# Kernel tuning notes

Hardware: AMD Instinct MI355X
Metric: run time of the kernel (lower is better)

Reference implementation:

```python
import jax, jax.numpy as jnp
import numpy as np
from jax import lax

B, T, E, K = 64, 512, 2048, 32


def setup_inputs() -> dict:
    key = jax.random.key(0)
    ks = jax.random.split(key, 8)
    X = jax.random.normal(ks[0], (B, T, E), dtype=jnp.float32)
    y = jax.random.randint(ks[1], (B, T), 0, K, dtype=jnp.int32)
    # variable-length mask: lengths in [T//2, T], position 0 always valid
    lengths = jax.random.randint(ks[2], (B,), T // 2, T + 1)
    mask = (jnp.arange(T)[None, :] < lengths[:, None])
    W = jax.random.normal(ks[3], (E, K), dtype=jnp.float32) * 0.02
    b = jnp.zeros((K,), dtype=jnp.float32)
    transitions = jax.random.normal(ks[4], (K, K), dtype=jnp.float32) * 0.1
    start_transitions = jax.random.normal(ks[5], (K,), dtype=jnp.float32) * 0.1
    end_transitions = jax.random.normal(ks[6], (K,), dtype=jnp.float32) * 0.1
    return {"X": X, "y": y, "mask": mask, "W": W, "b": b,
            "transitions": transitions,
            "start_transitions": start_transitions,
            "end_transitions": end_transitions}


def _input_likelihood(logits, mask, trans, start, end):
    # forward algorithm (log partition), AllenNLP semantics
    lt = jnp.transpose(logits, (1, 0, 2))  # [T,B,K]
    mt = mask.T                            # [T,B]
    alpha0 = start[None, :] + lt[0]        # [B,K]

    def step(alpha, xm):
        x, m = xm  # x:[B,K], m:[B]
        inner = alpha[:, :, None] + trans[None, :, :] + x[:, None, :]  # [B,K,K]
        new = jax.nn.logsumexp(inner, axis=1)
        return jnp.where(m[:, None], new, alpha), None

    alpha, _ = lax.scan(step, alpha0, (lt[1:], mt[1:]))
    return jax.nn.logsumexp(alpha + end[None, :], axis=1)  # [B]


def _joint_likelihood(logits, tags, mask, trans, start, end):
    maskf = mask.astype(logits.dtype)
    emit = jnp.take_along_axis(logits, tags[:, :, None], axis=2)[:, :, 0]  # [B,T]
    emit_score = jnp.sum(emit * maskf, axis=1)
    trans_sc = trans[tags[:, :-1], tags[:, 1:]]  # [B,T-1]
    trans_score = jnp.sum(trans_sc * maskf[:, 1:], axis=1)
    lengths = jnp.sum(mask.astype(jnp.int32), axis=1)
    last_tags = jnp.take_along_axis(tags, (lengths - 1)[:, None], axis=1)[:, 0]
    return start[tags[:, 0]] + emit_score + trans_score + end[last_tags]


def reference(X, y, mask, W, b, transitions, start_transitions, end_transitions):
    logits = jnp.einsum('bte,ek->btk', X, W) + b  # projection
    log_num = _joint_likelihood(logits, y, mask, transitions,
                                start_transitions, end_transitions)
    log_den = _input_likelihood(logits, mask, transitions,
                                start_transitions, end_transitions)
    # CRF.forward training path: loss = -crf(inputs, tags, mask)
    return -jnp.sum(log_num - log_den)
```

## Files before the change

kernel.cpp:

```cpp
#include <hip/hip_runtime.h>

#define Bn 64
#define Tn 512
#define En 2048
#define Kn 32
#define Mn (Bn*Tn)
#define LOG2E 1.4426950408889634f
#define LN2   0.6931471805599453f

typedef __attribute__((ext_vector_type(8))) short short8;
typedef __attribute__((ext_vector_type(4))) float floatx4;

__device__ inline unsigned int pack_bf16(float a, float b) {
    unsigned int ua = __float_as_uint(a), ub = __float_as_uint(b);
    return ((ua + 0x8000u) >> 16) | (((ub + 0x8000u) & 0xFFFF0000u));
}

__device__ inline float rdlane(float v, int l) {
    return __uint_as_float(__builtin_amdgcn_readlane(__float_as_uint(v), l));
}

__global__ __launch_bounds__(256) void prep_kernel(const float* __restrict__ W,
                                                   unsigned short* __restrict__ Wt,
                                                   float* __restrict__ out) {
    int idx = blockIdx.x * 256 + threadIdx.x;
    int k = idx >> 11, e = idx & 2047;
    float w = W[e * Kn + k];
    Wt[idx] = (unsigned short)((__float_as_uint(w) + 0x8000u) >> 16);
    if (idx == 0) out[0] = 0.f;
}

__global__ __launch_bounds__(256) void gemm_kernel(const float* __restrict__ X,
                                                   const float* __restrict__ bias,
                                                   const unsigned short* __restrict__ Wt,
                                                   float* __restrict__ logits2) {
    const int tid  = threadIdx.x;
    const int wave = tid >> 6;
    const int lane = tid & 63;
    const int ml   = lane & 15;
    const int quad = lane >> 4;
    const int row0 = blockIdx.x * 64;

    const float*          xp  = X  + (size_t)(row0 + wave * 16 + ml) * En + quad * 8;
    const unsigned short* b0p = Wt + ml * En        + quad * 8;
    const unsigned short* b1p = Wt + (16 + ml) * En + quad * 8;

    floatx4 acc0 = {0.f,0.f,0.f,0.f};
    floatx4 acc1 = {0.f,0.f,0.f,0.f};

    #pragma unroll 4
    for (int e0 = 0; e0 < En; e0 += 32) {
        float4 xa = *(const float4*)(xp + e0);
        float4 xb = *(const float4*)(xp + e0 + 4);
        short8 b0 = *(const short8*)(b0p + e0);
        short8 b1 = *(const short8*)(b1p + e0);
        union { unsigned int u[4]; short8 s; } av;
        av.u[0] = pack_bf16(xa.x, xa.y);
        av.u[1] = pack_bf16(xa.z, xa.w);
        av.u[2] = pack_bf16(xb.x, xb.y);
        av.u[3] = pack_bf16(xb.z, xb.w);
        acc0 = __builtin_amdgcn_mfma_f32_16x16x32_bf16(av.s, b0, acc0, 0, 0, 0);
        acc1 = __builtin_amdgcn_mfma_f32_16x16x32_bf16(av.s, b1, acc1, 0, 0, 0);
    }

    const float bc0 = bias[ml], bc1 = bias[16 + ml];
    const int gr = row0 + wave * 16 + quad * 4;
    #pragma unroll
    for (int r = 0; r < 4; ++r) {
        logits2[(size_t)(gr + r) * Kn + ml]      = (acc0[r] + bc0) * LOG2E;
        logits2[(size_t)(gr + r) * Kn + 16 + ml] = (acc1[r] + bc1) * LOG2E;
    }
}

__global__ __launch_bounds__(64) void crf_kernel(const float* __restrict__ logits2,
                                                 const int* __restrict__ y,
                                                 const void* __restrict__ maskp,
                                                 const float* __restrict__ trans,
                                                 const float* __restrict__ start,
                                                 const float* __restrict__ endt,
                                                 float* __restrict__ out) {
    const int b    = blockIdx.x;
    const int lane = threadIdx.x;
    const int j    = lane & 31;

    unsigned int first = *(const unsigned int*)maskp;
    int mode;
    if (first <= 1u) mode = 0;
    else if (first == 0x3F800000u) mode = 2;
    else mode = 1;

    int len = 0;
    if (mode == 0) {
        const int* mb = (const int*)maskp + b * Tn;
        for (int t = lane; t < Tn; t += 64) len += (mb[t] != 0);
    } else if (mode == 1) {
        const unsigned char* mb = (const unsigned char*)maskp + b * Tn;
        for (int t = lane; t < Tn; t += 64) len += (mb[t] != 0);
    } else {
        const float* mb = (const float*)maskp + b * Tn;
        for (int t = lane; t < Tn; t += 64) len += (mb[t] != 0.f);
    }
    #pragma unroll
    for (int o = 32; o; o >>= 1) len += __shfl_xor(len, o, 64);

    const int* yb = y + b * Tn;
    float num2 = 0.f;
    for (int t = lane; t < Tn; t += 64) {
        if (t < len) {
            int yt = yb[t];
            num2 += logits2[((size_t)b * Tn + t) * Kn + yt];
            if (t >= 1) num2 += trans[yb[t - 1] * Kn + yt] * LOG2E;
        }
    }
    if (lane == 0) num2 += (start[yb[0]] + endt[yb[len - 1]]) * LOG2E;
    #pragma unroll
    for (int o = 32; o; o >>= 1) num2 += __shfl_xor(num2, o, 64);

    float P[32];
    #pragma unroll
    for (int i = 0; i < 32; ++i)
        P[i] = __builtin_exp2f(trans[i * Kn + j] * LOG2E);

    const float* xrow = logits2 + (size_t)b * Tn * Kn;
    float a = start[j] * LOG2E + xrow[j];
    float S = 0.f;

    float cur[4], nxt[4];
    #pragma unroll
    for (int q = 0; q < 4; ++q) {
        int tq = 1 + q; if (tq > Tn - 1) tq = Tn - 1;
        cur[q] = xrow[tq * Kn + j];
    }

    for (int g = 1; g < len; g += 4) {
        #pragma unroll
        for (int q = 0; q < 4; ++q) {
            int tq = g + 4 + q; if (tq > Tn - 1) tq = Tn - 1;
            nxt[q] = xrow[tq * Kn + j];
        }
        #pragma unroll
        for (int q = 0; q < 4; ++q) {
            if (g + q < len) {
                float u = __builtin_exp2f(a);
                float w0 = 0.f, w1 = 0.f, w2 = 0.f, w3 = 0.f;
                #pragma unroll
                for (int i = 0; i < 32; i += 4) {
                    float s0 = rdlane(u, i);
                    float s1 = rdlane(u, i + 1);
                    float s2 = rdlane(u, i + 2);
                    float s3 = rdlane(u, i + 3);
                    w0 = fmaf(s0, P[i],     w0);
                    w1 = fmaf(s1, P[i + 1], w1);
                    w2 = fmaf(s2, P[i + 2], w2);
                    w3 = fmaf(s3, P[i + 3], w3);
                }
                float w = (w0 + w1) + (w2 + w3);
                float n = cur[q] + __builtin_log2f(w);
                if (q == 3) {
                    float sg = rdlane(n, 0);
                    a = n - sg;
                    S += sg;
                } else {
                    a = n;
                }
            }
        }
        #pragma unroll
        for (int q = 0; q < 4; ++q) cur[q] = nxt[q];
    }

    float v = (lane < 32) ? __builtin_exp2f(a + endt[j] * LOG2E) : 0.f;
    #pragma unroll
    for (int o = 32; o; o >>= 1) v += __shfl_xor(v, o, 64);
    float den2 = S + __builtin_log2f(v);

    if (lane == 0) atomicAdd(out, (den2 - num2) * LN2);
}

extern "C" void kernel_launch(void* const* d_in, const int* in_sizes, int n_in,
                              void* d_out, int out_size, void* d_ws, size_t ws_size,
                              hipStream_t stream) {
    const float* X     = (const float*)d_in[0];
    const int*   y     = (const int*)  d_in[1];
    const void*  mask  =               d_in[2];
    const float* W     = (const float*)d_in[3];
    const float* bias  = (const float*)d_in[4];
    const float* trans = (const float*)d_in[5];
    const float* start = (const float*)d_in[6];
    const float* endt  = (const float*)d_in[7];
    float* out = (float*)d_out;

    float* logits2 = (float*)d_ws;
    unsigned short* Wt = (unsigned short*)((char*)d_ws + (size_t)Mn * Kn * 4);

    prep_kernel<<<256, 256, 0, stream>>>(W, Wt, out);
    gemm_kernel<<<Mn / 64, 256, 0, stream>>>(X, bias, Wt, logits2);
    crf_kernel<<<Bn, 64, 0, stream>>>(logits2, y, mask, trans, start, endt, out);
}
```

Measured before the change: 466.7 us.

## Parallelize CRF forward recursion over time segments via MFMA transfer-matrix products

Splits each sequence's forward recursion into 8 segments of 64 steps. Each segment computes the product of its per-step 32x32 transfer matrices with bf16 MFMA, applying periodic exponent rescaling, and a combine kernel chains the segment matrices into the alpha vector. This turns a serial 512-step chain over 64 blocks into 512 blocks each running a shorter chain, exposing more parallelism. The cost is extra matrix-product work and bf16 truncation of intermediate products, which may affect accuracy. The GEMM unroll is also raised from 4 to 8.

```diff
diff --git a/kernel.cpp b/kernel.cpp
--- a/kernel.cpp
+++ b/kernel.cpp
@@ -7,15 +7,20 @@
 #define Mn (Bn*Tn)
 #define LOG2E 1.4426950408889634f
 #define LN2   0.6931471805599453f
-
-typedef __attribute__((ext_vector_type(8))) short short8;
-typedef __attribute__((ext_vector_type(4))) float floatx4;
+#define NSEG 8
+#define SEGLEN 64
+
+typedef __attribute__((ext_vector_type(8)))  short short8;
+typedef __attribute__((ext_vector_type(4)))  float floatx4;
+typedef __attribute__((ext_vector_type(16))) float floatx16;
 
 __device__ inline unsigned int pack_bf16(float a, float b) {
     unsigned int ua = __float_as_uint(a), ub = __float_as_uint(b);
     return ((ua + 0x8000u) >> 16) | (((ub + 0x8000u) & 0xFFFF0000u));
 }
-
+__device__ inline unsigned int pack_trunc(float lo, float hi) {
+    return (__float_as_uint(lo) >> 16) | (__float_as_uint(hi) & 0xFFFF0000u);
+}
 __device__ inline float rdlane(float v, int l) {
     return __uint_as_float(__builtin_amdgcn_readlane(__float_as_uint(v), l));
 }
@@ -48,7 +53,7 @@
     floatx4 acc0 = {0.f,0.f,0.f,0.f};
     floatx4 acc1 = {0.f,0.f,0.f,0.f};
 
-    #pragma unroll 4
+    #pragma unroll 8
     for (int e0 = 0; e0 < En; e0 += 32) {
         float4 xa = *(const float4*)(xp + e0);
         float4 xb = *(const float4*)(xp + e0 + 4);
@@ -72,23 +77,9 @@
     }
 }
 
-__global__ __launch_bounds__(64) void crf_kernel(const float* __restrict__ logits2,
-                                                 const int* __restrict__ y,
-                                                 const void* __restrict__ maskp,
-                                                 const float* __restrict__ trans,
-                                                 const float* __restrict__ start,
-                                                 const float* __restrict__ endt,
-                                                 float* __restrict__ out) {
-    const int b    = blockIdx.x;
-    const int lane = threadIdx.x;
-    const int j    = lane & 31;
-
+__device__ inline int seq_len(const void* maskp, int b, int lane) {
     unsigned int first = *(const unsigned int*)maskp;
-    int mode;
-    if (first <= 1u) mode = 0;
-    else if (first == 0x3F800000u) mode = 2;
-    else mode = 1;
-
+    int mode = (first <= 1u) ? 0 : (first == 0x3F800000u ? 2 : 1);
     int len = 0;
     if (mode == 0) {
         const int* mb = (const int*)maskp + b * Tn;
@@ -102,6 +93,124 @@
     }
     #pragma unroll
     for (int o = 32; o; o >>= 1) len += __shfl_xor(len, o, 64);
+    return len;
+}
+
+__global__ __launch_bounds__(64) void crf_seg_kernel(const float* __restrict__ logits2,
+                                                     const void* __restrict__ maskp,
+                                                     const float* __restrict__ trans,
+                                                     float* __restrict__ Hs,
+                                                     float* __restrict__ Ss) {
+    const int bx = blockIdx.x;
+    const int b = bx >> 3, s = bx & 7;
+    const int lane = threadIdx.x;
+    const int j = lane & 31;
+    const int h = lane >> 5;
+
+    const int len = seq_len(maskp, b, lane);
+    if (s * SEGLEN >= len) return;
+    const int tstart = (s == 0) ? 1 : s * SEGLEN;
+    const int tend   = min(s * SEGLEN + SEGLEN - 1, len - 1);
+
+    float PT1[8], PT2[8];
+    #pragma unroll
+    for (int i = 0; i < 8; ++i) {
+        PT1[i] = __builtin_exp2f(trans[(8 * h + i) * Kn + j] * LOG2E);
+        PT2[i] = __builtin_exp2f(trans[(16 + 8 * h + i) * Kn + j] * LOG2E);
+    }
+
+    union U4 { unsigned int u[4]; short8 v; };
+    U4 fb1, fb2;
+    #pragma unroll
+    for (int p = 0; p < 4; ++p) { fb1.u[p] = 0u; fb2.u[p] = 0u; }
+    int i1 = j - 8 * h;
+    if (i1 >= 0 && i1 < 8) fb1.u[i1 >> 1] |= 0x3F80u << (16 * (i1 & 1));
+    int i2 = j - 16 - 8 * h;
+    if (i2 >= 0 && i2 < 8) fb2.u[i2 >> 1] |= 0x3F80u << (16 * (i2 & 1));
+
+    const float* xrow = logits2 + (size_t)b * Tn * Kn + j;
+    floatx16 Hc;
+    float S = 0.f;
+    int stepc = 0;
+
+    float cur[4], nxt[4];
+    #pragma unroll
+    for (int q = 0; q < 4; ++q) cur[q] = xrow[min(tstart + q, tend) * Kn];
+
+    for (int g = tstart; g <= tend; g += 4) {
+        #pragma unroll
+        for (int q = 0; q < 4; ++q) nxt[q] = xrow[min(g + 4 + q, tend) * Kn];
+        #pragma unroll
+        for (int q = 0; q < 4; ++q) {
+            if (g + q <= tend) {
+                float e = __builtin_exp2f(cur[q]);
+                U4 fa1, fa2;
+                #pragma unroll
+                for (int p = 0; p < 4; ++p) {
+                    fa1.u[p] = pack_trunc(e * PT1[2 * p], e * PT1[2 * p + 1]);
+                    fa2.u[p] = pack_trunc(e * PT2[2 * p], e * PT2[2 * p + 1]);
+                }
+                floatx16 acc = {0.f,0.f,0.f,0.f,0.f,0.f,0.f,0.f,
+                                0.f,0.f,0.f,0.f,0.f,0.f,0.f,0.f};
+                acc = __builtin_amdgcn_mfma_f32_32x32x16_bf16(fa1.v, fb1.v, acc, 0, 0, 0);
+                acc = __builtin_amdgcn_mfma_f32_32x32x16_bf16(fa2.v, fb2.v, acc, 0, 0, 0);
+
+                if ((stepc & 7) == 7) {
+                    float m = acc[0];
+                    #pragma unroll
+                    for (int r = 1; r < 16; ++r) m = fmaxf(m, acc[r]);
+                    #pragma unroll
+                    for (int o = 1; o < 64; o <<= 1) m = fmaxf(m, __shfl_xor(m, o, 64));
+                    int eb = (int)((__float_as_uint(m) >> 23) & 0xFF);
+                    float scale = __uint_as_float((unsigned int)(254 - eb) << 23);
+                    #pragma unroll
+                    for (int r = 0; r < 16; ++r) acc[r] *= scale;
+                    S += (float)(eb - 127);
+                }
+                ++stepc;
+                Hc = acc;
+
+                unsigned int w[8], pw[8];
+                #pragma unroll
+                for (int p = 0; p < 8; ++p) w[p] = pack_trunc(acc[2 * p], acc[2 * p + 1]);
+                #pragma unroll
+                for (int p = 0; p < 8; ++p) pw[p] = __shfl_xor(w[p], 32, 64);
+                if (h == 0) {
+                    fb1.u[0] = w[0];  fb1.u[1] = w[1];  fb1.u[2] = pw[0]; fb1.u[3] = pw[1];
+                    fb2.u[0] = w[4];  fb2.u[1] = w[5];  fb2.u[2] = pw[4]; fb2.u[3] = pw[5];
+                } else {
+                    fb1.u[0] = pw[2]; fb1.u[1] = pw[3]; fb1.u[2] = w[2];  fb1.u[3] = w[3];
+                    fb2.u[0] = pw[6]; fb2.u[1] = pw[7]; fb2.u[2] = w[6];  fb2.u[3] = w[7];
+                }
+            }
+        }
+        #pragma unroll
+        for (int q = 0; q < 4; ++q) cur[q] = nxt[q];
+    }
+
+    float* hp = Hs + (size_t)(b * 8 + s) * 1024;
+    #pragma unroll
+    for (int r = 0; r < 16; ++r) {
+        int row = (r & 3) + 8 * (r >> 2) + 4 * h;
+        hp[row * 32 + j] = Hc[r];
+    }
+    if (lane == 0) Ss[b * 8 + s] = S;
+}
+
+__global__ __launch_bounds__(64) void crf_comb_kernel(const float* __restrict__ logits2,
+                                                      const int* __restrict__ y,
+                                                      const void* __restrict__ maskp,
+                                                      const float* __restrict__ trans,
+                                                      const float* __restrict__ start,
+                                                      const float* __restrict__ endt,
+                                                      const float* __restrict__ Hs,
+                                                      const float* __restrict__ Ss,
+                                                      float* __restrict__ out) {
+    const int b = blockIdx.x;
+    const int lane = threadIdx.x;
+    const int j = lane & 31;
+
+    const int len = seq_len(maskp, b, lane);
 
     const int* yb = y + b * Tn;
     float num2 = 0.f;
@@ -116,63 +225,40 @@
     #pragma unroll
     for (int o = 32; o; o >>= 1) num2 += __shfl_xor(num2, o, 64);
 
-    float P[32];
-    #pragma unroll
-    for (int i = 0; i < 32; ++i)
-        P[i] = __builtin_exp2f(trans[i * Kn + j] * LOG2E);
-
-    const float* xrow = logits2 + (size_t)b * Tn * Kn;
-    float a = start[j] * LOG2E + xrow[j];
-    float S = 0.f;
-
-    float cur[4], nxt[4];
-    #pragma unroll
-    for (int q = 0; q < 4; ++q) {
-        int tq = 1 + q; if (tq > Tn - 1) tq = Tn - 1;
-        cur[q] = xrow[tq * Kn + j];
-    }
-
-    for (int g = 1; g < len; g += 4) {
-        #pragma unroll
-        for (int q = 0; q < 4; ++q) {
-            int tq = g + 4 + q; if (tq > Tn - 1) tq = Tn - 1;
-            nxt[q] = xrow[tq * Kn + j];
+    float a2 = start[j] * LOG2E + logits2[(size_t)b * Tn * Kn + j];
+    float m0 = a2;
+    #pragma unroll
+    for (int o = 1; o < 64; o <<= 1) m0 = fmaxf(m0, __shfl_xor(m0, o, 64));
+    float S = m0;
+    float u = __builtin_exp2f(a2 - m0);
+
+    for (int s = 0; s < NSEG; ++s) {
+        if (s * SEGLEN >= len) break;
+        const float* hrow = Hs + (size_t)(b * 8 + s) * 1024 + j * 32;
+        float4 hr[8];
+        #pragma unroll
+        for (int p = 0; p < 8; ++p) hr[p] = *(const float4*)(hrow + 4 * p);
+        float v0 = 0.f, v1 = 0.f, v2 = 0.f, v3 = 0.f;
+        #pragma unroll
+        for (int p = 0; p < 8; ++p) {
+            v0 = fmaf(hr[p].x, rdlane(u, 4 * p),     v0);
+            v1 = fmaf(hr[p].y, rdlane(u, 4 * p + 1), v1);
+            v2 = fmaf(hr[p].z, rdlane(u, 4 * p + 2), v2);
+            v3 = fmaf(hr[p].w, rdlane(u, 4 * p + 3), v3);
         }
-        #pragma unroll
-        for (int q = 0; q < 4; ++q) {
-            if (g + q < len) {
-                float u = __builtin_exp2f(a);
-                float w0 = 0.f, w1 = 0.f, w2 = 0.f, w3 = 0.f;
-                #pragma unroll
-                for (int i = 0; i < 32; i += 4) {
-                    float s0 = rdlane(u, i);
-                    float s1 = rdlane(u, i + 1);
-                    float s2 = rdlane(u, i + 2);
-                    float s3 = rdlane(u, i + 3);
-                    w0 = fmaf(s0, P[i],     w0);
-                    w1 = fmaf(s1, P[i + 1], w1);
-                    w2 = fmaf(s2, P[i + 2], w2);
-                    w3 = fmaf(s3, P[i + 3], w3);
-                }
-                float w = (w0 + w1) + (w2 + w3);
-                float n = cur[q] + __builtin_log2f(w);
-                if (q == 3) {
-                    float sg = rdlane(n, 0);
-                    a = n - sg;
-                    S += sg;
-                } else {
-                    a = n;
-                }
-            }
-        }
-        #pragma unroll
-        for (int q = 0; q < 4; ++q) cur[q] = nxt[q];
-    }
-
-    float v = (lane < 32) ? __builtin_exp2f(a + endt[j] * LOG2E) : 0.f;
-    #pragma unroll
-    for (int o = 32; o; o >>= 1) v += __shfl_xor(v, o, 64);
-    float den2 = S + __builtin_log2f(v);
+        float v = (v0 + v1) + (v2 + v3);
+        float mm = v;
+        #pragma unroll
+        for (int o = 1; o < 64; o <<= 1) mm = fmaxf(mm, __shfl_xor(mm, o, 64));
+        int eb = (int)((__float_as_uint(mm) >> 23) & 0xFF);
+        u = v * __uint_as_float((unsigned int)(254 - eb) << 23);
+        S += (float)(eb - 127) + Ss[b * 8 + s];
+    }
+
+    float fv = (lane < 32) ? u * __builtin_exp2f(endt[j] * LOG2E) : 0.f;
+    #pragma unroll
+    for (int o = 32; o; o >>= 1) fv += __shfl_xor(fv, o, 64);
+    float den2 = S + __builtin_log2f(fv);
 
     if (lane == 0) atomicAdd(out, (den2 - num2) * LN2);
 }
@@ -190,10 +276,14 @@
     const float* endt  = (const float*)d_in[7];
     float* out = (float*)d_out;
 
-    float* logits2 = (float*)d_ws;
-    unsigned short* Wt = (unsigned short*)((char*)d_ws + (size_t)Mn * Kn * 4);
+    char* ws = (char*)d_ws;
+    float*          logits2 = (float*)ws;                         ws += (size_t)Mn * Kn * 4;
+    unsigned short* Wt      = (unsigned short*)ws;                ws += (size_t)Kn * En * 2;
+    float*          Hs      = (float*)ws;                         ws += (size_t)Bn * NSEG * 1024 * 4;
+    float*          Ss      = (float*)ws;
 
     prep_kernel<<<256, 256, 0, stream>>>(W, Wt, out);
     gemm_kernel<<<Mn / 64, 256, 0, stream>>>(X, bias, Wt, logits2);
-    crf_kernel<<<Bn, 64, 0, stream>>>(logits2, y, mask, trans, start, endt, out);
-}
+    crf_seg_kernel<<<Bn * NSEG, 64, 0, stream>>>(logits2, mask, trans, Hs, Ss);
+    crf_comb_kernel<<<Bn, 64, 0, stream>>>(logits2, y, mask, trans, start, endt, Hs, Ss, out);
+}
```

New measurement: 431.9 us. 7.4% less time.
